# Kernel optimization log

Measured on AMD Instinct MI355X. Metric: run time of the kernel, lower is better.

The kernel has to match this reference:

```python
import jax, jax.numpy as jnp
import numpy as np

N_ROIS = 512
N_EDGES = N_ROIS * N_ROIS
N_VIEWS = 6
DIMS = [(1, 36), (36, 24), (24, 5)]  # (in, out) for conv1..3


def _init_params(key):
    params = []
    for li, (cin, cout) in enumerate(DIMS):
        k = jax.random.fold_in(key, li)
        k1, k2, k3 = jax.random.split(k, 3)
        lw = jax.random.normal(k1, (N_VIEWS, cin * cout), dtype=jnp.float32) * 0.1
        lb = jnp.zeros((cin * cout,), dtype=jnp.float32)
        root = jax.random.normal(k2, (cin, cout), dtype=jnp.float32) * 0.1
        b = jnp.zeros((cout,), dtype=jnp.float32)
        params += [lw, lb, root, b]
    return params


def setup_inputs() -> dict:
    key = jax.random.key(0)
    k1, k2, k3 = jax.random.split(key, 3)
    x = jnp.ones((N_ROIS, 1), dtype=jnp.float32)
    edge_attr = jax.random.uniform(k1, (N_EDGES, N_VIEWS), dtype=jnp.float32)
    edge_index = jax.random.randint(k2, (2, N_EDGES), 0, N_ROIS, dtype=jnp.int64)
    p = _init_params(k3)
    names = []
    for i in (1, 2, 3):
        names += [f"lw{i}", f"lb{i}", f"root{i}", f"b{i}"]
    out = {"x": x, "edge_attr": edge_attr, "edge_index": edge_index}
    out.update(dict(zip(names, p)))
    return out


def _nnconv(x, edge_index, edge_attr, lw, lb, root, b, cin, cout):
    # Edge MLP: Linear + ReLU -> per-edge weight matrix [E, cin, cout]
    w = jax.nn.relu(edge_attr @ lw + lb).reshape(-1, cin, cout)
    src, dst = edge_index[0], edge_index[1]
    # gather source node features, per-edge matmul
    msg = jnp.einsum('ei,eio->eo', x[src], w)  # [E, cout]
    ssum = jax.ops.segment_sum(msg, dst, num_segments=N_ROIS)
    cnt = jax.ops.segment_sum(jnp.ones((msg.shape[0],), dtype=x.dtype), dst,
                              num_segments=N_ROIS)
    aggr = ssum / jnp.maximum(cnt, 1.0)[:, None]  # mean aggregation
    return aggr + x @ root + b  # root weight + bias (PyG NNConv defaults)


def reference(x, edge_attr, edge_index,
              lw1, lb1, root1, b1,
              lw2, lb2, root2, b2,
              lw3, lb3, root3, b3):
    h = jax.nn.relu(_nnconv(x, edge_index, edge_attr, lw1, lb1, root1, b1, *DIMS[0]))
    h = jax.nn.relu(_nnconv(h, edge_index, edge_attr, lw2, lb2, root2, b2, *DIMS[1]))
    h = jax.nn.relu(_nnconv(h, edge_index, edge_attr, lw3, lb3, root3, b3, *DIMS[2]))
    # cbt[i, j] = sum_k |h[i,k] - h[j,k]|  (repeat/transpose/abs/sum tail)
    cbt = jnp.sum(jnp.abs(h[:, None, :] - h[None, :, :]), axis=2)  # [N, N]
    return cbt
```

## Files before the change

### kernel.cpp

```cpp
#include <hip/hip_runtime.h>

#define NROIS 512
#define NEDGES 262144

__device__ __forceinline__ int detect_i64(const unsigned* __restrict__ er) {
    unsigned acc = 0;
#pragma unroll
    for (int i = 0; i < 64; ++i) acc |= er[2 * i + 1];
    return acc == 0u;
}

__device__ __forceinline__ void load_edge(const unsigned* __restrict__ er,
                                          bool i64, int e, int& src, int& dst) {
    if (i64) { src = (int)er[2 * e]; dst = (int)er[2 * NEDGES + 2 * e]; }
    else     { src = (int)er[e];     dst = (int)er[NEDGES + e]; }
}

__global__ __launch_bounds__(256) void hist_kernel(const unsigned* __restrict__ er,
                                                   int* __restrict__ gpart)
{
    __shared__ int lh[NROIS];
    __shared__ int s_l;
    const int t = threadIdx.x;
    if (t == 0) s_l = detect_i64(er);
    for (int i = t; i < NROIS; i += 256) lh[i] = 0;
    __syncthreads();
    const bool L = (s_l != 0);
    const int e0 = blockIdx.x * 4096;
#pragma unroll
    for (int k = 0; k < 16; ++k) {
        int e = e0 + k * 256 + t, src, dst;
        load_edge(er, L, e, src, dst);
        atomicAdd(&lh[dst], 1);
    }
    __syncthreads();
    for (int i = t; i < NROIS; i += 256) gpart[blockIdx.x * NROIS + i] = lh[i];
}

__global__ __launch_bounds__(512) void scan_kernel(const int* __restrict__ gpart,
                                                   int* __restrict__ start,
                                                   int* __restrict__ cursor)
{
    __shared__ int tmp[NROIS];
    const int t = threadIdx.x;
    int own = 0;
#pragma unroll 8
    for (int b = 0; b < 64; ++b) own += gpart[b * NROIS + t];
    tmp[t] = own;
    __syncthreads();
    for (int off = 1; off < NROIS; off <<= 1) {
        int v = tmp[t];
        int add = (t >= off) ? tmp[t - off] : 0;
        __syncthreads();
        tmp[t] = v + add;
        __syncthreads();
    }
    start[t + 1] = tmp[t];
    if (t == 0) start[0] = 0;
    cursor[t] = tmp[t] - own;
}

__global__ __launch_bounds__(256) void scatter_kernel(const unsigned* __restrict__ er,
                                                      const float* __restrict__ ea,
                                                      int* __restrict__ gcursor,
                                                      unsigned* __restrict__ perm,
                                                      float* __restrict__ eas,
                                                      int packed)
{
    __shared__ int lh[NROIS];
    __shared__ int lbase[NROIS];
    __shared__ int s_l;
    const int t = threadIdx.x;
    if (t == 0) s_l = detect_i64(er);
    for (int i = t; i < NROIS; i += 256) lh[i] = 0;
    __syncthreads();
    const bool L = (s_l != 0);
    const int e0 = blockIdx.x * 1024;
#pragma unroll
    for (int k = 0; k < 4; ++k) {
        int e = e0 + k * 256 + t, src, dst;
        load_edge(er, L, e, src, dst);
        atomicAdd(&lh[dst], 1);
    }
    __syncthreads();
    for (int i = t; i < NROIS; i += 256) {
        int c = lh[i];
        lbase[i] = c ? atomicAdd(&gcursor[i], c) : 0;
    }
    __syncthreads();
#pragma unroll
    for (int k = 0; k < 4; ++k) {
        int e = e0 + k * 256 + t, src, dst;
        load_edge(er, L, e, src, dst);
        int pos = atomicAdd(&lbase[dst], 1);
        unsigned ps = ((unsigned)e << 9) | (unsigned)src;
        perm[pos] = ps;
        if (packed) {
            const float2* s = reinterpret_cast<const float2*>(ea + (size_t)e * 6);
            const float2 a0 = s[0], a1 = s[1], a2 = s[2];
            float4* d = reinterpret_cast<float4*>(eas + (size_t)pos * 8);
            d[0] = make_float4(a0.x, a0.y, a1.x, a1.y);
            d[1] = make_float4(a2.x, a2.y, __uint_as_float(ps), 0.f);
        }
    }
}

template <int CIN, int COUT, int NP, int BLOCK, int SPLIT, bool PACKED>
__global__ __launch_bounds__(BLOCK) void edge_aggr_kernel(
    const float* __restrict__ eas, const float* __restrict__ ea,
    const unsigned* __restrict__ perm, const int* __restrict__ start,
    const float* __restrict__ lw, const float* __restrict__ lb,
    const float* __restrict__ hin, float* __restrict__ partial)
{
    constexpr int OGRP = COUT / NP;
    constexpr int TUSED = CIN * OGRP;
    const int t = threadIdx.x;
    const int tc = (t < TUSED) ? t : 0;
    const int ii = tc / OGRP, og = tc % OGRP;

    float wb[NP], wv[NP][6];
#pragma unroll
    for (int p = 0; p < NP; ++p) {
        const int o = og * NP + p;
        wb[p] = lb[ii * COUT + o];
#pragma unroll
        for (int v = 0; v < 6; ++v) wv[p][v] = lw[v * (CIN * COUT) + ii * COUT + o];
    }

    const int dst = blockIdx.y, chunk = blockIdx.x;
    const int s0 = start[dst];
    const int cnt = start[dst + 1] - s0;
    const int c0 = s0 + (cnt * chunk) / SPLIT;
    const int c1 = s0 + (cnt * (chunk + 1)) / SPLIT;

    float acc[NP];
#pragma unroll
    for (int p = 0; p < NP; ++p) acc[p] = 0.f;

#pragma unroll 4
    for (int idx = c0; idx < c1; ++idx) {
        float a0, a1, a2, a3, a4, a5;
        unsigned ps;
        if constexpr (PACKED) {
            const float* __restrict__ ap = eas + (size_t)idx * 8;
            a0 = ap[0]; a1 = ap[1]; a2 = ap[2]; a3 = ap[3]; a4 = ap[4]; a5 = ap[5];
            ps = __float_as_uint(ap[6]);
        } else {
            ps = perm[idx];
            const float* __restrict__ ap = ea + (size_t)(ps >> 9) * 6;
            a0 = ap[0]; a1 = ap[1]; a2 = ap[2]; a3 = ap[3]; a4 = ap[4]; a5 = ap[5];
        }
        const int src = (int)(ps & 511u);
        const float hsv = hin[src * CIN + ii];
#pragma unroll
        for (int p = 0; p < NP; ++p) {
            float tt = wb[p];
            tt = fmaf(a0, wv[p][0], tt);
            tt = fmaf(a1, wv[p][1], tt);
            tt = fmaf(a2, wv[p][2], tt);
            tt = fmaf(a3, wv[p][3], tt);
            tt = fmaf(a4, wv[p][4], tt);
            tt = fmaf(a5, wv[p][5], tt);
            acc[p] = fmaf(hsv, fmaxf(tt, 0.f), acc[p]);
        }
    }

    float* __restrict__ out = partial + ((size_t)chunk * NROIS + dst) * COUT;
    if constexpr (CIN == 1) {
        if (t < COUT) out[t] = acc[0];
    } else {
        __shared__ float red[CIN * COUT];
        if (t < TUSED) {
#pragma unroll
            for (int p = 0; p < NP; ++p) red[ii * COUT + og * NP + p] = acc[p];
        }
        __syncthreads();
        if (t < COUT) {
            float tot = 0.f;
#pragma unroll 4
            for (int k = 0; k < CIN; ++k) tot += red[k * COUT + t];
            out[t] = tot;
        }
    }
}

template <int CIN, int COUT, int SPLIT>
__global__ __launch_bounds__(256) void node_kernel(
    const float* __restrict__ hin, const float* __restrict__ partial,
    const int* __restrict__ start, const float* __restrict__ root,
    const float* __restrict__ bias, float* __restrict__ hout)
{
    int t = blockIdx.x * 256 + threadIdx.x;
    if (t >= NROIS * COUT) return;
    int i = t / COUT, o = t - i * COUT;
    float s = 0.f;
#pragma unroll
    for (int c = 0; c < SPLIT; ++c) s += partial[((size_t)c * NROIS + i) * COUT + o];
    int cnt = start[i + 1] - start[i];
    float aggr = s / fmaxf((float)cnt, 1.f);
    float r = bias[o];
#pragma unroll 4
    for (int k = 0; k < CIN; ++k) r = fmaf(hin[i * CIN + k], root[k * COUT + o], r);
    hout[t] = fmaxf(aggr + r, 0.f);
}

__global__ __launch_bounds__(256) void cbt_kernel(const float* __restrict__ h,
                                                  float* __restrict__ out)
{
    __shared__ float sh[NROIS * 5];
    for (int t = threadIdx.x; t < NROIS * 5; t += 256) sh[t] = h[t];
    __syncthreads();
    const int i = blockIdx.x;
    float hi[5];
#pragma unroll
    for (int k = 0; k < 5; ++k) hi[k] = sh[i * 5 + k];
    for (int j = threadIdx.x; j < NROIS; j += 256) {
        float s = 0.f;
#pragma unroll
        for (int k = 0; k < 5; ++k) s += fabsf(hi[k] - sh[j * 5 + k]);
        out[i * NROIS + j] = s;
    }
}

extern "C" void kernel_launch(void* const* d_in, const int* in_sizes, int n_in,
                              void* d_out, int out_size, void* d_ws, size_t ws_size,
                              hipStream_t stream)
{
    const float*    x     = (const float*)d_in[0];
    const float*    ea    = (const float*)d_in[1];
    const unsigned* er    = (const unsigned*)d_in[2];
    const float*    lw1   = (const float*)d_in[3];
    const float*    lb1   = (const float*)d_in[4];
    const float*    root1 = (const float*)d_in[5];
    const float*    b1    = (const float*)d_in[6];
    const float*    lw2   = (const float*)d_in[7];
    const float*    lb2   = (const float*)d_in[8];
    const float*    root2 = (const float*)d_in[9];
    const float*    b2    = (const float*)d_in[10];
    const float*    lw3   = (const float*)d_in[11];
    const float*    lb3   = (const float*)d_in[12];
    const float*    root3 = (const float*)d_in[13];
    const float*    b3    = (const float*)d_in[14];

    const size_t easN  = (size_t)NEDGES * 8;
    const size_t restN = 18432 + 12288 + 2560 + 147456 + 513 + 512 + NEDGES;
    const size_t needPacked = (easN + restN) * 4;
    const int packed = (ws_size >= needPacked) ? 1 : 0;

    float* ws   = (float*)d_ws;
    float* eas  = ws;
    float* rest = packed ? (ws + easN) : ws;
    float* h1   = rest;
    float* h2   = h1 + NROIS * 36;
    float* h3   = h2 + NROIS * 24;
    float* part = h3 + NROIS * 5;
    int* gpart  = (int*)part;
    int* start  = (int*)(part + 147456);
    int* cursor = start + NROIS + 1;
    unsigned* perm = (unsigned*)(cursor + NROIS);

    hist_kernel<<<NEDGES / 4096, 256, 0, stream>>>(er, gpart);
    scan_kernel<<<1, 512, 0, stream>>>(gpart, start, cursor);
    scatter_kernel<<<NEDGES / 1024, 256, 0, stream>>>(er, ea, cursor, perm, eas, packed);

    if (packed) {
        edge_aggr_kernel<1, 36, 1, 64, 8, true><<<dim3(8, NROIS), 64, 0, stream>>>(
            eas, ea, perm, start, lw1, lb1, x, part);
        node_kernel<1, 36, 8><<<(NROIS * 36 + 255) / 256, 256, 0, stream>>>(
            x, part, start, root1, b1, h1);
        edge_aggr_kernel<36, 24, 8, 128, 8, true><<<dim3(8, NROIS), 128, 0, stream>>>(
            eas, ea, perm, start, lw2, lb2, h1, part);
        node_kernel<36, 24, 8><<<(NROIS * 24 + 255) / 256, 256, 0, stream>>>(
            h1, part, start, root2, b2, h2);
        edge_aggr_kernel<24, 5, 1, 128, 8, true><<<dim3(8, NROIS), 128, 0, stream>>>(
            eas, ea, perm, start, lw3, lb3, h2, part);
        node_kernel<24, 5, 8><<<(NROIS * 5 + 255) / 256, 256, 0, stream>>>(
            h2, part, start, root3, b3, h3);
    } else {
        edge_aggr_kernel<1, 36, 1, 64, 8, false><<<dim3(8, NROIS), 64, 0, stream>>>(
            eas, ea, perm, start, lw1, lb1, x, part);
        node_kernel<1, 36, 8><<<(NROIS * 36 + 255) / 256, 256, 0, stream>>>(
            x, part, start, root1, b1, h1);
        edge_aggr_kernel<36, 24, 8, 128, 8, false><<<dim3(8, NROIS), 128, 0, stream>>>(
            eas, ea, perm, start, lw2, lb2, h1, part);
        node_kernel<36, 24, 8><<<(NROIS * 24 + 255) / 256, 256, 0, stream>>>(
            h1, part, start, root2, b2, h2);
        edge_aggr_kernel<24, 5, 1, 128, 8, false><<<dim3(8, NROIS), 128, 0, stream>>>(
            eas, ea, perm, start, lw3, lb3, h2, part);
        node_kernel<24, 5, 8><<<(NROIS * 5 + 255) / 256, 256, 0, stream>>>(
            h2, part, start, root3, b3, h3);
    }

    cbt_kernel<<<NROIS, 256, 0, stream>>>(h3, (float*)d_out);
}
```

Baseline: 139.7 us.

## Spread edges across thread groups in layers 1 and 3, vectorize packed edge loads

```diff
diff --git a/kernel.cpp b/kernel.cpp
--- a/kernel.cpp
+++ b/kernel.cpp
@@ -26,9 +26,9 @@
     for (int i = t; i < NROIS; i += 256) lh[i] = 0;
     __syncthreads();
     const bool L = (s_l != 0);
-    const int e0 = blockIdx.x * 4096;
-#pragma unroll
-    for (int k = 0; k < 16; ++k) {
+    const int e0 = blockIdx.x * 1024;
+#pragma unroll
+    for (int k = 0; k < 4; ++k) {
         int e = e0 + k * 256 + t, src, dst;
         load_edge(er, L, e, src, dst);
         atomicAdd(&lh[dst], 1);
@@ -45,7 +45,7 @@
     const int t = threadIdx.x;
     int own = 0;
 #pragma unroll 8
-    for (int b = 0; b < 64; ++b) own += gpart[b * NROIS + t];
+    for (int b = 0; b < 256; ++b) own += gpart[b * NROIS + t];
     tmp[t] = own;
     __syncthreads();
     for (int off = 1; off < NROIS; off <<= 1) {
@@ -105,8 +105,38 @@
     }
 }
 
+template <bool PACKED>
+__device__ __forceinline__ void fetch_edge(const float* __restrict__ eas,
+                                           const float* __restrict__ ea,
+                                           const unsigned* __restrict__ perm,
+                                           int idx, float a[6], unsigned& ps)
+{
+    if constexpr (PACKED) {
+        const float4* ap4 = reinterpret_cast<const float4*>(eas + (size_t)idx * 8);
+        const float4 r0 = ap4[0], r1 = ap4[1];
+        a[0] = r0.x; a[1] = r0.y; a[2] = r0.z; a[3] = r0.w;
+        a[4] = r1.x; a[5] = r1.y; ps = __float_as_uint(r1.z);
+    } else {
+        ps = perm[idx];
+        const float* ap = ea + (size_t)(ps >> 9) * 6;
+        a[0] = ap[0]; a[1] = ap[1]; a[2] = ap[2];
+        a[3] = ap[3]; a[4] = ap[4]; a[5] = ap[5];
+    }
+}
+
+__device__ __forceinline__ float edge_w(const float a[6], float wb, const float wv[6]) {
+    float tt = wb;
+    tt = fmaf(a[0], wv[0], tt);
+    tt = fmaf(a[1], wv[1], tt);
+    tt = fmaf(a[2], wv[2], tt);
+    tt = fmaf(a[3], wv[3], tt);
+    tt = fmaf(a[4], wv[4], tt);
+    tt = fmaf(a[5], wv[5], tt);
+    return fmaxf(tt, 0.f);
+}
+
 template <int CIN, int COUT, int NP, int BLOCK, int SPLIT, bool PACKED>
-__global__ __launch_bounds__(BLOCK) void edge_aggr_kernel(
+__global__ __launch_bounds__(BLOCK, 4) void edge_aggr_kernel(
     const float* __restrict__ eas, const float* __restrict__ ea,
     const unsigned* __restrict__ perm, const int* __restrict__ start,
     const float* __restrict__ lw, const float* __restrict__ lb,
@@ -137,50 +167,127 @@
 #pragma unroll
     for (int p = 0; p < NP; ++p) acc[p] = 0.f;
 
-#pragma unroll 4
+#pragma unroll 2
     for (int idx = c0; idx < c1; ++idx) {
-        float a0, a1, a2, a3, a4, a5;
-        unsigned ps;
-        if constexpr (PACKED) {
-            const float* __restrict__ ap = eas + (size_t)idx * 8;
-            a0 = ap[0]; a1 = ap[1]; a2 = ap[2]; a3 = ap[3]; a4 = ap[4]; a5 = ap[5];
-            ps = __float_as_uint(ap[6]);
-        } else {
-            ps = perm[idx];
-            const float* __restrict__ ap = ea + (size_t)(ps >> 9) * 6;
-            a0 = ap[0]; a1 = ap[1]; a2 = ap[2]; a3 = ap[3]; a4 = ap[4]; a5 = ap[5];
-        }
+        float a[6]; unsigned ps;
+        fetch_edge<PACKED>(eas, ea, perm, idx, a, ps);
         const int src = (int)(ps & 511u);
         const float hsv = hin[src * CIN + ii];
 #pragma unroll
-        for (int p = 0; p < NP; ++p) {
-            float tt = wb[p];
-            tt = fmaf(a0, wv[p][0], tt);
-            tt = fmaf(a1, wv[p][1], tt);
-            tt = fmaf(a2, wv[p][2], tt);
-            tt = fmaf(a3, wv[p][3], tt);
-            tt = fmaf(a4, wv[p][4], tt);
-            tt = fmaf(a5, wv[p][5], tt);
-            acc[p] = fmaf(hsv, fmaxf(tt, 0.f), acc[p]);
-        }
-    }
-
+        for (int p = 0; p < NP; ++p)
+            acc[p] = fmaf(hsv, edge_w(a, wb[p], wv[p]), acc[p]);
+    }
+
+    __shared__ float red[CIN * COUT];
+    if (t < TUSED) {
+#pragma unroll
+        for (int p = 0; p < NP; ++p) red[ii * COUT + og * NP + p] = acc[p];
+    }
+    __syncthreads();
     float* __restrict__ out = partial + ((size_t)chunk * NROIS + dst) * COUT;
-    if constexpr (CIN == 1) {
-        if (t < COUT) out[t] = acc[0];
-    } else {
-        __shared__ float red[CIN * COUT];
-        if (t < TUSED) {
-#pragma unroll
-            for (int p = 0; p < NP; ++p) red[ii * COUT + og * NP + p] = acc[p];
-        }
-        __syncthreads();
-        if (t < COUT) {
-            float tot = 0.f;
+    if (t < COUT) {
+        float tot = 0.f;
 #pragma unroll 4
-            for (int k = 0; k < CIN; ++k) tot += red[k * COUT + t];
-            out[t] = tot;
-        }
+        for (int k = 0; k < CIN; ++k) tot += red[k * COUT + t];
+        out[t] = tot;
+    }
+}
+
+template <int COUT, int G, int BLOCK, int SPLIT, bool PACKED>
+__global__ __launch_bounds__(BLOCK, 4) void edge_aggr1_kernel(
+    const float* __restrict__ eas, const float* __restrict__ ea,
+    const unsigned* __restrict__ perm, const int* __restrict__ start,
+    const float* __restrict__ lw, const float* __restrict__ lb,
+    const float* __restrict__ hin, float* __restrict__ partial)
+{
+    constexpr int TUSED = G * COUT;
+    const int t = threadIdx.x;
+    const int tc = (t < TUSED) ? t : 0;
+    const int g = tc / COUT, o = tc % COUT;
+
+    float wb = lb[o], wv[6];
+#pragma unroll
+    for (int v = 0; v < 6; ++v) wv[v] = lw[v * COUT + o];
+
+    const int dst = blockIdx.y, chunk = blockIdx.x;
+    const int s0 = start[dst];
+    const int cnt = start[dst + 1] - s0;
+    const int c0 = s0 + (cnt * chunk) / SPLIT;
+    const int c1 = s0 + (cnt * (chunk + 1)) / SPLIT;
+
+    float acc = 0.f;
+#pragma unroll 2
+    for (int idx = c0 + g; idx < c1; idx += G) {
+        float a[6]; unsigned ps;
+        fetch_edge<PACKED>(eas, ea, perm, idx, a, ps);
+        const float hsv = hin[(int)(ps & 511u)];
+        acc = fmaf(hsv, edge_w(a, wb, wv), acc);
+    }
+
+    __shared__ float red[TUSED];
+    if (t < TUSED) red[t] = acc;
+    __syncthreads();
+    float* __restrict__ out = partial + ((size_t)chunk * NROIS + dst) * COUT;
+    if (t < COUT) {
+        float tot = 0.f;
+#pragma unroll
+        for (int k = 0; k < G; ++k) tot += red[k * COUT + t];
+        out[t] = tot;
+    }
+}
+
+template <int CIN, int COUT, int G, int BLOCK, int SPLIT, bool PACKED>
+__global__ __launch_bounds__(BLOCK, 4) void edge_aggr3_kernel(
+    const float* __restrict__ eas, const float* __restrict__ ea,
+    const unsigned* __restrict__ perm, const int* __restrict__ start,
+    const float* __restrict__ lw, const float* __restrict__ lb,
+    const float* __restrict__ hin, float* __restrict__ partial)
+{
+    constexpr int TUSED = G * CIN;
+    const int t = threadIdx.x;
+    const int tc = (t < TUSED) ? t : 0;
+    const int g = tc / CIN, ii = tc % CIN;
+
+    float wb[COUT], wv[COUT][6];
+#pragma unroll
+    for (int o = 0; o < COUT; ++o) {
+        wb[o] = lb[ii * COUT + o];
+#pragma unroll
+        for (int v = 0; v < 6; ++v) wv[o][v] = lw[v * (CIN * COUT) + ii * COUT + o];
+    }
+
+    const int dst = blockIdx.y, chunk = blockIdx.x;
+    const int s0 = start[dst];
+    const int cnt = start[dst + 1] - s0;
+    const int c0 = s0 + (cnt * chunk) / SPLIT;
+    const int c1 = s0 + (cnt * (chunk + 1)) / SPLIT;
+
+    float acc[COUT];
+#pragma unroll
+    for (int o = 0; o < COUT; ++o) acc[o] = 0.f;
+
+#pragma unroll 2
+    for (int idx = c0 + g; idx < c1; idx += G) {
+        float a[6]; unsigned ps;
+        fetch_edge<PACKED>(eas, ea, perm, idx, a, ps);
+        const float hsv = hin[(int)(ps & 511u) * CIN + ii];
+#pragma unroll
+        for (int o = 0; o < COUT; ++o)
+            acc[o] = fmaf(hsv, edge_w(a, wb[o], wv[o]), acc[o]);
+    }
+
+    __shared__ float red[TUSED * COUT];
+    if (t < TUSED) {
+#pragma unroll
+        for (int o = 0; o < COUT; ++o) red[tc * COUT + o] = acc[o];
+    }
+    __syncthreads();
+    float* __restrict__ out = partial + ((size_t)chunk * NROIS + dst) * COUT;
+    if (t < COUT) {
+        float tot = 0.f;
+#pragma unroll 8
+        for (int k = 0; k < TUSED; ++k) tot += red[k * COUT + t];
+        out[t] = tot;
     }
 }
 
@@ -220,6 +327,29 @@
         for (int k = 0; k < 5; ++k) s += fabsf(hi[k] - sh[j * 5 + k]);
         out[i * NROIS + j] = s;
     }
+}
+
+template <bool PACKED>
+static void run_layers(const float* x, const float* ea, const unsigned* er,
+                       const float* lw1, const float* lb1, const float* root1, const float* b1,
+                       const float* lw2, const float* lb2, const float* root2, const float* b2,
+                       const float* lw3, const float* lb3, const float* root3, const float* b3,
+                       const float* eas, const unsigned* perm, const int* start,
+                       float* part, float* h1, float* h2, float* h3,
+                       hipStream_t stream)
+{
+    edge_aggr1_kernel<36, 7, 256, 8, PACKED><<<dim3(8, NROIS), 256, 0, stream>>>(
+        eas, ea, perm, start, lw1, lb1, x, part);
+    node_kernel<1, 36, 8><<<(NROIS * 36 + 255) / 256, 256, 0, stream>>>(
+        x, part, start, root1, b1, h1);
+    edge_aggr_kernel<36, 24, 8, 128, 8, PACKED><<<dim3(8, NROIS), 128, 0, stream>>>(
+        eas, ea, perm, start, lw2, lb2, h1, part);
+    node_kernel<36, 24, 8><<<(NROIS * 24 + 255) / 256, 256, 0, stream>>>(
+        h1, part, start, root2, b2, h2);
+    edge_aggr3_kernel<24, 5, 5, 128, 8, PACKED><<<dim3(8, NROIS), 128, 0, stream>>>(
+        eas, ea, perm, start, lw3, lb3, h2, part);
+    node_kernel<24, 5, 8><<<(NROIS * 5 + 255) / 256, 256, 0, stream>>>(
+        h2, part, start, root3, b3, h3);
 }
 
 extern "C" void kernel_launch(void* const* d_in, const int* in_sizes, int n_in,
@@ -259,37 +389,16 @@
     int* cursor = start + NROIS + 1;
     unsigned* perm = (unsigned*)(cursor + NROIS);
 
-    hist_kernel<<<NEDGES / 4096, 256, 0, stream>>>(er, gpart);
+    hist_kernel<<<NEDGES / 1024, 256, 0, stream>>>(er, gpart);
     scan_kernel<<<1, 512, 0, stream>>>(gpart, start, cursor);
     scatter_kernel<<<NEDGES / 1024, 256, 0, stream>>>(er, ea, cursor, perm, eas, packed);
 
-    if (packed) {
-        edge_aggr_kernel<1, 36, 1, 64, 8, true><<<dim3(8, NROIS), 64, 0, stream>>>(
-            eas, ea, perm, start, lw1, lb1, x, part);
-        node_kernel<1, 36, 8><<<(NROIS * 36 + 255) / 256, 256, 0, stream>>>(
-            x, part, start, root1, b1, h1);
-        edge_aggr_kernel<36, 24, 8, 128, 8, true><<<dim3(8, NROIS), 128, 0, stream>>>(
-            eas, ea, perm, start, lw2, lb2, h1, part);
-        node_kernel<36, 24, 8><<<(NROIS * 24 + 255) / 256, 256, 0, stream>>>(
-            h1, part, start, root2, b2, h2);
-        edge_aggr_kernel<24, 5, 1, 128, 8, true><<<dim3(8, NROIS), 128, 0, stream>>>(
-            eas, ea, perm, start, lw3, lb3, h2, part);
-        node_kernel<24, 5, 8><<<(NROIS * 5 + 255) / 256, 256, 0, stream>>>(
-            h2, part, start, root3, b3, h3);
-    } else {
-        edge_aggr_kernel<1, 36, 1, 64, 8, false><<<dim3(8, NROIS), 64, 0, stream>>>(
-            eas, ea, perm, start, lw1, lb1, x, part);
-        node_kernel<1, 36, 8><<<(NROIS * 36 + 255) / 256, 256, 0, stream>>>(
-            x, part, start, root1, b1, h1);
-        edge_aggr_kernel<36, 24, 8, 128, 8, false><<<dim3(8, NROIS), 128, 0, stream>>>(
-            eas, ea, perm, start, lw2, lb2, h1, part);
-        node_kernel<36, 24, 8><<<(NROIS * 24 + 255) / 256, 256, 0, stream>>>(
-            h1, part, start, root2, b2, h2);
-        edge_aggr_kernel<24, 5, 1, 128, 8, false><<<dim3(8, NROIS), 128, 0, stream>>>(
-            eas, ea, perm, start, lw3, lb3, h2, part);
-        node_kernel<24, 5, 8><<<(NROIS * 5 + 255) / 256, 256, 0, stream>>>(
-            h2, part, start, root3, b3, h3);
-    }
+    if (packed)
+        run_layers<true>(x, ea, er, lw1, lb1, root1, b1, lw2, lb2, root2, b2,
+                         lw3, lb3, root3, b3, eas, perm, start, part, h1, h2, h3, stream);
+    else
+        run_layers<false>(x, ea, er, lw1, lb1, root1, b1, lw2, lb2, root2, b2,
+                          lw3, lb3, root3, b3, eas, perm, start, part, h1, h2, h3, stream);
 
     cbt_kernel<<<NROIS, 256, 0, stream>>>(h3, (float*)d_out);
 }
```

Result: no change. 139.4 us (-0.2%).

## Fuse edge aggregation and node update into one per-destination layer kernel

Applied to the files above, without the earlier changes.

```diff
diff --git a/kernel.cpp b/kernel.cpp
--- a/kernel.cpp
+++ b/kernel.cpp
@@ -94,114 +94,99 @@
         load_edge(er, L, e, src, dst);
         int pos = atomicAdd(&lbase[dst], 1);
         unsigned ps = ((unsigned)e << 9) | (unsigned)src;
-        perm[pos] = ps;
         if (packed) {
             const float2* s = reinterpret_cast<const float2*>(ea + (size_t)e * 6);
             const float2 a0 = s[0], a1 = s[1], a2 = s[2];
             float4* d = reinterpret_cast<float4*>(eas + (size_t)pos * 8);
             d[0] = make_float4(a0.x, a0.y, a1.x, a1.y);
             d[1] = make_float4(a2.x, a2.y, __uint_as_float(ps), 0.f);
+        } else {
+            perm[pos] = ps;
         }
     }
 }
 
-template <int CIN, int COUT, int NP, int BLOCK, int SPLIT, bool PACKED>
-__global__ __launch_bounds__(BLOCK) void edge_aggr_kernel(
+template <int CIN, int COUT, int STR, bool PACKED>
+__global__ __launch_bounds__(256) void layer_kernel(
     const float* __restrict__ eas, const float* __restrict__ ea,
     const unsigned* __restrict__ perm, const int* __restrict__ start,
     const float* __restrict__ lw, const float* __restrict__ lb,
-    const float* __restrict__ hin, float* __restrict__ partial)
-{
-    constexpr int OGRP = COUT / NP;
-    constexpr int TUSED = CIN * OGRP;
-    const int t = threadIdx.x;
-    const int tc = (t < TUSED) ? t : 0;
-    const int ii = tc / OGRP, og = tc % OGRP;
-
-    float wb[NP], wv[NP][6];
-#pragma unroll
-    for (int p = 0; p < NP; ++p) {
-        const int o = og * NP + p;
-        wb[p] = lb[ii * COUT + o];
-#pragma unroll
-        for (int v = 0; v < 6; ++v) wv[p][v] = lw[v * (CIN * COUT) + ii * COUT + o];
-    }
-
-    const int dst = blockIdx.y, chunk = blockIdx.x;
-    const int s0 = start[dst];
-    const int cnt = start[dst + 1] - s0;
-    const int c0 = s0 + (cnt * chunk) / SPLIT;
-    const int c1 = s0 + (cnt * (chunk + 1)) / SPLIT;
-
-    float acc[NP];
-#pragma unroll
-    for (int p = 0; p < NP; ++p) acc[p] = 0.f;
-
-#pragma unroll 4
-    for (int idx = c0; idx < c1; ++idx) {
+    const float* __restrict__ root, const float* __restrict__ bias,
+    const float* __restrict__ hin, float* __restrict__ hout)
+{
+    __shared__ float sh[NROIS * STR];
+    __shared__ float red[4 * COUT];
+    const int t = threadIdx.x;
+
+    for (int idx = t; idx < NROIS * CIN; idx += 256) {
+        const int r = idx / CIN;
+        sh[r * STR + (idx - r * CIN)] = hin[idx];
+    }
+    __syncthreads();
+
+    const int dst = blockIdx.x;
+    const int s0 = start[dst], c1 = start[dst + 1];
+    const int cnt = c1 - s0;
+
+    float acc[COUT];
+#pragma unroll
+    for (int o = 0; o < COUT; ++o) acc[o] = 0.f;
+
+    for (int idx = s0 + t; idx < c1; idx += 256) {
         float a0, a1, a2, a3, a4, a5;
         unsigned ps;
         if constexpr (PACKED) {
-            const float* __restrict__ ap = eas + (size_t)idx * 8;
-            a0 = ap[0]; a1 = ap[1]; a2 = ap[2]; a3 = ap[3]; a4 = ap[4]; a5 = ap[5];
-            ps = __float_as_uint(ap[6]);
+            const float4* __restrict__ base = reinterpret_cast<const float4*>(eas);
+            const float4 r0 = base[2 * idx], r1 = base[2 * idx + 1];
+            a0 = r0.x; a1 = r0.y; a2 = r0.z; a3 = r0.w;
+            a4 = r1.x; a5 = r1.y; ps = __float_as_uint(r1.z);
         } else {
             ps = perm[idx];
             const float* __restrict__ ap = ea + (size_t)(ps >> 9) * 6;
             a0 = ap[0]; a1 = ap[1]; a2 = ap[2]; a3 = ap[3]; a4 = ap[4]; a5 = ap[5];
         }
-        const int src = (int)(ps & 511u);
-        const float hsv = hin[src * CIN + ii];
-#pragma unroll
-        for (int p = 0; p < NP; ++p) {
-            float tt = wb[p];
-            tt = fmaf(a0, wv[p][0], tt);
-            tt = fmaf(a1, wv[p][1], tt);
-            tt = fmaf(a2, wv[p][2], tt);
-            tt = fmaf(a3, wv[p][3], tt);
-            tt = fmaf(a4, wv[p][4], tt);
-            tt = fmaf(a5, wv[p][5], tt);
-            acc[p] = fmaf(hsv, fmaxf(tt, 0.f), acc[p]);
+        const int hbase = (int)(ps & 511u) * STR;
+
+#pragma unroll 2
+        for (int i = 0; i < CIN; ++i) {
+            const float hsv = sh[hbase + i];
+#pragma unroll
+            for (int o = 0; o < COUT; ++o) {
+                float tt = lb[i * COUT + o];
+                tt = fmaf(a0, lw[0 * (CIN * COUT) + i * COUT + o], tt);
+                tt = fmaf(a1, lw[1 * (CIN * COUT) + i * COUT + o], tt);
+                tt = fmaf(a2, lw[2 * (CIN * COUT) + i * COUT + o], tt);
+                tt = fmaf(a3, lw[3 * (CIN * COUT) + i * COUT + o], tt);
+                tt = fmaf(a4, lw[4 * (CIN * COUT) + i * COUT + o], tt);
+                tt = fmaf(a5, lw[5 * (CIN * COUT) + i * COUT + o], tt);
+                acc[o] = fmaf(hsv, fmaxf(tt, 0.f), acc[o]);
+            }
         }
     }
 
-    float* __restrict__ out = partial + ((size_t)chunk * NROIS + dst) * COUT;
-    if constexpr (CIN == 1) {
-        if (t < COUT) out[t] = acc[0];
-    } else {
-        __shared__ float red[CIN * COUT];
-        if (t < TUSED) {
-#pragma unroll
-            for (int p = 0; p < NP; ++p) red[ii * COUT + og * NP + p] = acc[p];
-        }
-        __syncthreads();
-        if (t < COUT) {
-            float tot = 0.f;
+#pragma unroll
+    for (int o = 0; o < COUT; ++o) {
+        float v = acc[o];
+#pragma unroll
+        for (int d = 32; d > 0; d >>= 1) v += __shfl_xor(v, d);
+        acc[o] = v;
+    }
+    const int lane = t & 63, wid = t >> 6;
+    if (lane == 0) {
+#pragma unroll
+        for (int o = 0; o < COUT; ++o) red[wid * COUT + o] = acc[o];
+    }
+    __syncthreads();
+
+    if (t < COUT) {
+        float tot = red[t] + red[COUT + t] + red[2 * COUT + t] + red[3 * COUT + t];
+        float aggr = tot / fmaxf((float)cnt, 1.f);
+        float r = bias[t];
 #pragma unroll 4
-            for (int k = 0; k < CIN; ++k) tot += red[k * COUT + t];
-            out[t] = tot;
-        }
-    }
-}
-
-template <int CIN, int COUT, int SPLIT>
-__global__ __launch_bounds__(256) void node_kernel(
-    const float* __restrict__ hin, const float* __restrict__ partial,
-    const int* __restrict__ start, const float* __restrict__ root,
-    const float* __restrict__ bias, float* __restrict__ hout)
-{
-    int t = blockIdx.x * 256 + threadIdx.x;
-    if (t >= NROIS * COUT) return;
-    int i = t / COUT, o = t - i * COUT;
-    float s = 0.f;
-#pragma unroll
-    for (int c = 0; c < SPLIT; ++c) s += partial[((size_t)c * NROIS + i) * COUT + o];
-    int cnt = start[i + 1] - start[i];
-    float aggr = s / fmaxf((float)cnt, 1.f);
-    float r = bias[o];
-#pragma unroll 4
-    for (int k = 0; k < CIN; ++k) r = fmaf(hin[i * CIN + k], root[k * COUT + o], r);
-    hout[t] = fmaxf(aggr + r, 0.f);
+        for (int k = 0; k < CIN; ++k)
+            r = fmaf(sh[dst * STR + k], root[k * COUT + t], r);
+        hout[dst * COUT + t] = fmaxf(aggr + r, 0.f);
+    }
 }
 
 __global__ __launch_bounds__(256) void cbt_kernel(const float* __restrict__ h,
@@ -220,6 +205,22 @@
         for (int k = 0; k < 5; ++k) s += fabsf(hi[k] - sh[j * 5 + k]);
         out[i * NROIS + j] = s;
     }
+}
+
+template <bool PACKED>
+static void run_layers(const float* x, const float* ea,
+                       const float* lw1, const float* lb1, const float* root1, const float* b1,
+                       const float* lw2, const float* lb2, const float* root2, const float* b2,
+                       const float* lw3, const float* lb3, const float* root3, const float* b3,
+                       const float* eas, const unsigned* perm, const int* start,
+                       float* h1, float* h2, float* h3, hipStream_t stream)
+{
+    layer_kernel<1, 36, 1, PACKED><<<NROIS, 256, 0, stream>>>(
+        eas, ea, perm, start, lw1, lb1, root1, b1, x, h1);
+    layer_kernel<36, 24, 37, PACKED><<<NROIS, 256, 0, stream>>>(
+        eas, ea, perm, start, lw2, lb2, root2, b2, h1, h2);
+    layer_kernel<24, 5, 25, PACKED><<<NROIS, 256, 0, stream>>>(
+        eas, ea, perm, start, lw3, lb3, root3, b3, h2, h3);
 }
 
 extern "C" void kernel_launch(void* const* d_in, const int* in_sizes, int n_in,
@@ -243,7 +244,7 @@
     const float*    b3    = (const float*)d_in[14];
 
     const size_t easN  = (size_t)NEDGES * 8;
-    const size_t restN = 18432 + 12288 + 2560 + 147456 + 513 + 512 + NEDGES;
+    const size_t restN = 18432 + 12288 + 2560 + 131072 + 513 + 512 + NEDGES;
     const size_t needPacked = (easN + restN) * 4;
     const int packed = (ws_size >= needPacked) ? 1 : 0;
 
@@ -253,9 +254,8 @@
     float* h1   = rest;
     float* h2   = h1 + NROIS * 36;
     float* h3   = h2 + NROIS * 24;
-    float* part = h3 + NROIS * 5;
-    int* gpart  = (int*)part;
-    int* start  = (int*)(part + 147456);
+    int* gpart  = (int*)(h3 + NROIS * 5);
+    int* start  = gpart + 131072;
     int* cursor = start + NROIS + 1;
     unsigned* perm = (unsigned*)(cursor + NROIS);
 
@@ -263,33 +263,12 @@
     scan_kernel<<<1, 512, 0, stream>>>(gpart, start, cursor);
     scatter_kernel<<<NEDGES / 1024, 256, 0, stream>>>(er, ea, cursor, perm, eas, packed);
 
-    if (packed) {
-        edge_aggr_kernel<1, 36, 1, 64, 8, true><<<dim3(8, NROIS), 64, 0, stream>>>(
-            eas, ea, perm, start, lw1, lb1, x, part);
-        node_kernel<1, 36, 8><<<(NROIS * 36 + 255) / 256, 256, 0, stream>>>(
-            x, part, start, root1, b1, h1);
-        edge_aggr_kernel<36, 24, 8, 128, 8, true><<<dim3(8, NROIS), 128, 0, stream>>>(
-            eas, ea, perm, start, lw2, lb2, h1, part);
-        node_kernel<36, 24, 8><<<(NROIS * 24 + 255) / 256, 256, 0, stream>>>(
-            h1, part, start, root2, b2, h2);
-        edge_aggr_kernel<24, 5, 1, 128, 8, true><<<dim3(8, NROIS), 128, 0, stream>>>(
-            eas, ea, perm, start, lw3, lb3, h2, part);
-        node_kernel<24, 5, 8><<<(NROIS * 5 + 255) / 256, 256, 0, stream>>>(
-            h2, part, start, root3, b3, h3);
-    } else {
-        edge_aggr_kernel<1, 36, 1, 64, 8, false><<<dim3(8, NROIS), 64, 0, stream>>>(
-            eas, ea, perm, start, lw1, lb1, x, part);
-        node_kernel<1, 36, 8><<<(NROIS * 36 + 255) / 256, 256, 0, stream>>>(
-            x, part, start, root1, b1, h1);
-        edge_aggr_kernel<36, 24, 8, 128, 8, false><<<dim3(8, NROIS), 128, 0, stream>>>(
-            eas, ea, perm, start, lw2, lb2, h1, part);
-        node_kernel<36, 24, 8><<<(NROIS * 24 + 255) / 256, 256, 0, stream>>>(
-            h1, part, start, root2, b2, h2);
-        edge_aggr_kernel<24, 5, 1, 128, 8, false><<<dim3(8, NROIS), 128, 0, stream>>>(
-            eas, ea, perm, start, lw3, lb3, h2, part);
-        node_kernel<24, 5, 8><<<(NROIS * 5 + 255) / 256, 256, 0, stream>>>(
-            h2, part, start, root3, b3, h3);
-    }
+    if (packed)
+        run_layers<true>(x, ea, lw1, lb1, root1, b1, lw2, lb2, root2, b2,
+                         lw3, lb3, root3, b3, eas, perm, start, h1, h2, h3, stream);
+    else
+        run_layers<false>(x, ea, lw1, lb1, root1, b1, lw2, lb2, root2, b2,
+                          lw3, lb3, root3, b3, eas, perm, start, h1, h2, h3, stream);
 
     cbt_kernel<<<NROIS, 256, 0, stream>>>(h3, (float*)d_out);
 }
```

New measurement: 161.5 us. 15.6% more time.
